# Kernel optimization log

Hardware: AMD Instinct MI355X
Metric: run time of the kernel (lower is better)

The kernel has to match this reference:

```python
import jax, jax.numpy as jnp
import numpy as np

S, IN, OUT = 32, 2048, 2048


def setup_inputs() -> dict:
    key = jax.random.key(0)
    k1, k2, k3 = jax.random.split(key, 3)
    lim = 1.0 / np.sqrt(IN)
    return {
        "x": jax.random.normal(k1, (S, IN), dtype=jnp.float32),
        "weight_mu": jax.random.uniform(k2, (OUT, IN), dtype=jnp.float32, minval=-lim, maxval=lim),
        "weight_sigma": jnp.full((OUT, IN), 0.1, dtype=jnp.float32),
        "bias_mu": jax.random.uniform(k3, (OUT,), dtype=jnp.float32, minval=-lim, maxval=lim),
        "bias_sigma": jnp.full((OUT,), 0.1, dtype=jnp.float32),
        "samples": S,
    }


def reference(x, weight_mu, weight_sigma, bias_mu, bias_sigma, samples):
    # Reparameterized sampling: w = mu + sigma * eps, eps ~ N(0,1), one weight per sample.
    key = jax.random.key(42)
    wkey, bkey = jax.random.split(key)
    eps_w = jax.random.normal(wkey, (samples,) + weight_mu.shape, dtype=weight_mu.dtype)  # (S, OUT, IN)
    weights = weight_mu + weight_sigma * eps_w  # (S, OUT, IN)
    # Per-sample matvec: out[s] = weights[s] @ x[s]
    out = jnp.einsum("soi,si->so", weights, x)  # (S, OUT)
    eps_b = jax.random.normal(bkey, (samples,) + bias_mu.shape, dtype=bias_mu.dtype)  # (S, OUT)
    out = out + (bias_mu + bias_sigma * eps_b)
    return out
```

## Files before the change

### kernel.cpp

```cpp
#include <hip/hip_runtime.h>
#include <stdint.h>

#define NS 32
#define NIN 2048
#define NOUT 2048

__device__ __forceinline__ uint32_t rotl32(uint32_t v, uint32_t r) {
    return __builtin_amdgcn_alignbit(v, v, 32u - r);
}

#define TF_R(x0, x1, r)          \
    do {                         \
        x0 += x1;                \
        x1 = rotl32(x1, r) ^ x0; \
    } while (0)

__device__ __forceinline__ uint32_t tf_fold(uint32_t k0, uint32_t k1, uint32_t k2,
                                            uint32_t x1in) {
    uint32_t x0 = k0 + x1in;
    uint32_t x1 = rotl32(x1in, 13) ^ x0;
    TF_R(x0, x1, 15); TF_R(x0, x1, 26); TF_R(x0, x1, 6);
    x0 += k1; x1 += k2 + 1u;
    TF_R(x0, x1, 17); TF_R(x0, x1, 29); TF_R(x0, x1, 16); TF_R(x0, x1, 24);
    x0 += k2; x1 += k0 + 2u;
    TF_R(x0, x1, 13); TF_R(x0, x1, 15); TF_R(x0, x1, 26); TF_R(x0, x1, 6);
    x0 += k0; x1 += k1 + 3u;
    TF_R(x0, x1, 17); TF_R(x0, x1, 29); TF_R(x0, x1, 16); TF_R(x0, x1, 24);
    x0 += k1; x1 += k2 + 4u;
    TF_R(x0, x1, 13); TF_R(x0, x1, 15); TF_R(x0, x1, 26); TF_R(x0, x1, 6);
    x0 += k2; x1 += k0 + 5u;
    return x0 ^ x1;
}

__device__ __forceinline__ float normal_from_bits(uint32_t bits) {
    const float LO = __uint_as_float(0xBF7FFFFFu);
    float f = __uint_as_float((bits >> 9) | 0x3f800000u) - 1.0f;
    float u = fmaf(f, 2.0f, LO);
    float w = -__logf(fmaf(-u, u, 1.0f));
    float p;
    if (w < 5.0f) {
        w -= 2.5f;
        p = 2.81022636e-08f;
        p = fmaf(p, w, 3.43273939e-07f);
        p = fmaf(p, w, -3.5233877e-06f);
        p = fmaf(p, w, -4.39150654e-06f);
        p = fmaf(p, w, 0.00021858087f);
        p = fmaf(p, w, -0.00125372503f);
        p = fmaf(p, w, -0.00417768164f);
        p = fmaf(p, w, 0.246640727f);
        p = fmaf(p, w, 1.50140941f);
    } else {
        w = __fsqrt_rn(w) - 3.0f;
        p = -0.000200214257f;
        p = fmaf(p, w, 0.000100950558f);
        p = fmaf(p, w, 0.00134934322f);
        p = fmaf(p, w, -0.00367342844f);
        p = fmaf(p, w, 0.00573950773f);
        p = fmaf(p, w, -0.0076224613f);
        p = fmaf(p, w, 0.00943887047f);
        p = fmaf(p, w, 1.00167406f);
        p = fmaf(p, w, 2.83297682f);
    }
    return 1.41421356237f * p * u;
}

__global__ __launch_bounds__(256, 2) void bayes_linear_kernel(
    const float* __restrict__ x, const float* __restrict__ wmu,
    const float* __restrict__ wsg, const float* __restrict__ bmu,
    const float* __restrict__ bsg, float* __restrict__ out,
    uint32_t kw0, uint32_t kw1, uint32_t kb0, uint32_t kb1) {
    const int o = blockIdx.x;
    const int tid = threadIdx.x;

    const uint32_t kw2 = kw0 ^ kw1 ^ 0x1BD11BDAu;
    const uint32_t kb2 = kb0 ^ kb1 ^ 0x1BD11BDAu;

    float acc[NS];
#pragma unroll
    for (int s = 0; s < NS; ++s) acc[s] = 0.0f;

    const uint32_t baseo = (uint32_t)o * NIN;

    for (int j = 0; j < NIN; j += 256) {
        const int i = j + tid;
        const float mu = wmu[baseo + (uint32_t)i];
        const float sg = wsg[baseo + (uint32_t)i];
        const uint32_t pbk = baseo + (uint32_t)i + kw1;
#pragma unroll 8
        for (int s = 0; s < NS; ++s) {
            const uint32_t x1in = pbk + (uint32_t)s * (uint32_t)(NOUT * NIN);
            const float e = normal_from_bits(tf_fold(kw0, kw1, kw2, x1in));
            const float xs = x[s * NIN + i];
            acc[s] = fmaf(fmaf(sg, e, mu), xs, acc[s]);
        }
    }

    __shared__ float red[4][NS];
    const int lane = tid & 63;
    const int wv = tid >> 6;
#pragma unroll
    for (int s = 0; s < NS; ++s) {
        float v = acc[s];
        v += __shfl_down(v, 32, 64);
        v += __shfl_down(v, 16, 64);
        v += __shfl_down(v, 8, 64);
        v += __shfl_down(v, 4, 64);
        v += __shfl_down(v, 2, 64);
        v += __shfl_down(v, 1, 64);
        if (lane == 0) red[wv][s] = v;
    }
    __syncthreads();

    if (tid < NS) {
        const int s = tid;
        float sum = red[0][s] + red[1][s] + red[2][s] + red[3][s];
        const uint32_t pb = (uint32_t)(s * NOUT + o) + kb1;
        const float eb = normal_from_bits(tf_fold(kb0, kb1, kb2, pb));
        out[s * NOUT + o] = sum + fmaf(bsg[o], eb, bmu[o]);
    }
}

#define TF_ROUND_H(x0, x1, r)                     \
    do {                                          \
        x0 += x1;                                 \
        x1 = (x1 << (r)) | (x1 >> (32 - (r)));    \
        x1 ^= x0;                                 \
    } while (0)

static void tf2x32_host(uint32_t k0, uint32_t k1, uint32_t x0, uint32_t x1,
                        uint32_t* y0, uint32_t* y1) {
    uint32_t k2 = k0 ^ k1 ^ 0x1BD11BDAu;
    x0 += k0; x1 += k1;
    TF_ROUND_H(x0, x1, 13); TF_ROUND_H(x0, x1, 15); TF_ROUND_H(x0, x1, 26); TF_ROUND_H(x0, x1, 6);
    x0 += k1; x1 += k2 + 1u;
    TF_ROUND_H(x0, x1, 17); TF_ROUND_H(x0, x1, 29); TF_ROUND_H(x0, x1, 16); TF_ROUND_H(x0, x1, 24);
    x0 += k2; x1 += k0 + 2u;
    TF_ROUND_H(x0, x1, 13); TF_ROUND_H(x0, x1, 15); TF_ROUND_H(x0, x1, 26); TF_ROUND_H(x0, x1, 6);
    x0 += k0; x1 += k1 + 3u;
    TF_ROUND_H(x0, x1, 17); TF_ROUND_H(x0, x1, 29); TF_ROUND_H(x0, x1, 16); TF_ROUND_H(x0, x1, 24);
    x0 += k1; x1 += k2 + 4u;
    TF_ROUND_H(x0, x1, 13); TF_ROUND_H(x0, x1, 15); TF_ROUND_H(x0, x1, 26); TF_ROUND_H(x0, x1, 6);
    x0 += k2; x1 += k0 + 5u;
    *y0 = x0; *y1 = x1;
}

extern "C" void kernel_launch(void* const* d_in, const int* in_sizes, int n_in,
                              void* d_out, int out_size, void* d_ws, size_t ws_size,
                              hipStream_t stream) {
    const float* x   = (const float*)d_in[0];
    const float* wmu = (const float*)d_in[1];
    const float* wsg = (const float*)d_in[2];
    const float* bmu = (const float*)d_in[3];
    const float* bsg = (const float*)d_in[4];
    float* out = (float*)d_out;

    uint32_t kw0, kw1, kb0, kb1;
    tf2x32_host(0u, 42u, 0u, 0u, &kw0, &kw1);
    tf2x32_host(0u, 42u, 0u, 1u, &kb0, &kb1);

    bayes_linear_kernel<<<NOUT, 256, 0, stream>>>(x, wmu, wsg, bmu, bsg, out,
                                                  kw0, kw1, kb0, kb1);
}
```

Measured before the change: 312.2 us.

## Map threads to sample and contiguous input chunk, drop 32-way accumulator arrays

```diff
diff --git a/kernel.cpp b/kernel.cpp
--- a/kernel.cpp
+++ b/kernel.cpp
@@ -64,59 +64,59 @@
     return 1.41421356237f * p * u;
 }
 
-__global__ __launch_bounds__(256, 2) void bayes_linear_kernel(
+__global__ __launch_bounds__(256, 4) void bayes_linear_kernel(
     const float* __restrict__ x, const float* __restrict__ wmu,
     const float* __restrict__ wsg, const float* __restrict__ bmu,
     const float* __restrict__ bsg, float* __restrict__ out,
     uint32_t kw0, uint32_t kw1, uint32_t kb0, uint32_t kb1) {
     const int o = blockIdx.x;
     const int tid = threadIdx.x;
+    const int s = tid & 31;
+    const int g = tid >> 5;
 
     const uint32_t kw2 = kw0 ^ kw1 ^ 0x1BD11BDAu;
     const uint32_t kb2 = kb0 ^ kb1 ^ 0x1BD11BDAu;
 
-    float acc[NS];
-#pragma unroll
-    for (int s = 0; s < NS; ++s) acc[s] = 0.0f;
+    const uint32_t baseo = (uint32_t)o * NIN;
+    const uint32_t ibase = (uint32_t)g * (NIN / 8);
+    const uint32_t pb0 = (uint32_t)s * (uint32_t)(NOUT * NIN) + baseo + ibase + kw1;
 
-    const uint32_t baseo = (uint32_t)o * NIN;
+    const float4* __restrict__ wmu4 = (const float4*)(wmu + baseo + ibase);
+    const float4* __restrict__ wsg4 = (const float4*)(wsg + baseo + ibase);
+    const float4* __restrict__ xp4  = (const float4*)(x + (uint32_t)s * NIN + ibase);
 
-    for (int j = 0; j < NIN; j += 256) {
-        const int i = j + tid;
-        const float mu = wmu[baseo + (uint32_t)i];
-        const float sg = wsg[baseo + (uint32_t)i];
-        const uint32_t pbk = baseo + (uint32_t)i + kw1;
-#pragma unroll 8
-        for (int s = 0; s < NS; ++s) {
-            const uint32_t x1in = pbk + (uint32_t)s * (uint32_t)(NOUT * NIN);
-            const float e = normal_from_bits(tf_fold(kw0, kw1, kw2, x1in));
-            const float xs = x[s * NIN + i];
-            acc[s] = fmaf(fmaf(sg, e, mu), xs, acc[s]);
-        }
+    float acc0 = 0.0f, acc1 = 0.0f;
+    for (int it = 0; it < NIN / 8 / 4; ++it) {
+        const float4 m4 = wmu4[it];
+        const float4 g4 = wsg4[it];
+        const float4 xv = xp4[it];
+        const uint32_t p = pb0 + (uint32_t)(it * 4);
+        const uint32_t b0 = tf_fold(kw0, kw1, kw2, p + 0u);
+        const uint32_t b1 = tf_fold(kw0, kw1, kw2, p + 1u);
+        const uint32_t b2 = tf_fold(kw0, kw1, kw2, p + 2u);
+        const uint32_t b3 = tf_fold(kw0, kw1, kw2, p + 3u);
+        const float e0 = normal_from_bits(b0);
+        const float e1 = normal_from_bits(b1);
+        const float e2 = normal_from_bits(b2);
+        const float e3 = normal_from_bits(b3);
+        acc0 = fmaf(fmaf(g4.x, e0, m4.x), xv.x, acc0);
+        acc1 = fmaf(fmaf(g4.y, e1, m4.y), xv.y, acc1);
+        acc0 = fmaf(fmaf(g4.z, e2, m4.z), xv.z, acc0);
+        acc1 = fmaf(fmaf(g4.w, e3, m4.w), xv.w, acc1);
     }
 
-    __shared__ float red[4][NS];
-    const int lane = tid & 63;
-    const int wv = tid >> 6;
-#pragma unroll
-    for (int s = 0; s < NS; ++s) {
-        float v = acc[s];
-        v += __shfl_down(v, 32, 64);
-        v += __shfl_down(v, 16, 64);
-        v += __shfl_down(v, 8, 64);
-        v += __shfl_down(v, 4, 64);
-        v += __shfl_down(v, 2, 64);
-        v += __shfl_down(v, 1, 64);
-        if (lane == 0) red[wv][s] = v;
-    }
+    __shared__ float red[8][NS];
+    red[g][s] = acc0 + acc1;
     __syncthreads();
 
     if (tid < NS) {
-        const int s = tid;
-        float sum = red[0][s] + red[1][s] + red[2][s] + red[3][s];
-        const uint32_t pb = (uint32_t)(s * NOUT + o) + kb1;
+        const int ss = tid;
+        float sum = 0.0f;
+#pragma unroll
+        for (int gg = 0; gg < 8; ++gg) sum += red[gg][ss];
+        const uint32_t pb = (uint32_t)(ss * NOUT + o) + kb1;
         const float eb = normal_from_bits(tf_fold(kb0, kb1, kb2, pb));
-        out[s * NOUT + o] = sum + fmaf(bsg[o], eb, bmu[o]);
+        out[ss * NOUT + o] = sum + fmaf(bsg[o], eb, bmu[o]);
     }
 }
 
```

New measurement: 371.9 us. +19.1%, slower.
